# Performance work log

Hardware: AMD Instinct MI355X
Metric: run time of the kernel (lower is better)

## Reference

```python
import jax, jax.numpy as jnp
import numpy as np

N_NODES = 50000
N_EDGES = 1_600_000
F_IN = 128
F_OUT = 8
K_TAPS = 4
AVG_DEG = 32.0


def setup_inputs() -> dict:
    key = jax.random.key(0)
    k1, k2, k3, k4, k5 = jax.random.split(key, 5)
    x = jax.random.normal(k1, (N_NODES, F_IN), dtype=jnp.float32)
    gso_rows = jax.random.randint(k2, (N_EDGES,), 0, N_NODES, dtype=jnp.int32)
    gso_cols = jax.random.randint(k3, (N_EDGES,), 0, N_NODES, dtype=jnp.int32)
    gso_vals = jax.random.uniform(k4, (N_EDGES,), dtype=jnp.float32) / AVG_DEG
    # filterCoeff = randn(outFeat, filter_order) * 0.1 as in torch __init__
    coeff = jax.random.normal(k5, (F_OUT, K_TAPS), dtype=jnp.float32) * 0.1
    return {"x": x, "gso_rows": gso_rows, "gso_cols": gso_cols,
            "gso_vals": gso_vals, "coeff": coeff}


def reference(x, gso_rows, gso_cols, gso_vals, coeff):
    # Faithful to the torch code INCLUDING its carried-over SpMV state:
    # output feature o uses powers S^{1+o(K-1)} .. S^{o(K-1)+K} of x.
    F_out, K = coeff.shape
    N = x.shape[0]
    max_power = F_out * (K - 1) + 1  # highest S power needed

    def spmv(Z):  # S @ Z via edge-list gather + segment_sum scatter
        return jax.ops.segment_sum(gso_vals[:, None] * Z[gso_cols], gso_rows,
                                   num_segments=N)

    def step(Z, _):
        Zn = spmv(Z)
        return Zn, Zn.sum(axis=1)  # sum over in-features done up-front

    # s[p-1, n] = sum_f (S^p x)[n, f], for p = 1..max_power
    _, s = jax.lax.scan(step, x, None, length=max_power)  # (max_power, N)

    # power index (0-based into s) used by output o, tap i: o*(K-1) + i
    idx = jnp.arange(F_out)[:, None] * (K - 1) + jnp.arange(K)[None, :]  # (F_out, K)
    sg = s[idx]  # (F_out, K, N)
    y = jnp.einsum('ok,okn->no', coeff, sg)  # (N, F_out)
    return y
```

## Files before the change

kernel.cpp:

```cpp
#include <hip/hip_runtime.h>
#include <hip/hip_bf16.h>

#define N_NODES 50000
#define N_EDGES 1600000
#define F_IN    128
#define F_OUT   8
#define K_TAPS  4
#define MAX_POWER 25

#define NBLK    256
#define RPB     196
#define CHUNK   4096
#define NPART   391
#define ECAP_G  8192
#define ECAP_L  6912

#define BAR_LINES 16
#define LSTRIDE   32

__device__ inline int wave_incl_scan(int v, int lane) {
    #pragma unroll
    for (int off = 1; off < 64; off <<= 1) {
        int t = __shfl_up(v, off, 64);
        if (lane >= off) v += t;
    }
    return v;
}

__device__ inline void st_coh(float* p, float v) {
    __hip_atomic_store(p, v, __ATOMIC_RELAXED, __HIP_MEMORY_SCOPE_AGENT);
}

__global__ void partition_kernel(const int* __restrict__ rows,
                                 const int* __restrict__ cols,
                                 const float* __restrict__ vals,
                                 int* __restrict__ gcnt,
                                 int2* __restrict__ edges, int n_edges) {
    __shared__ int lhist[NBLK];
    __shared__ int lcur[NBLK];
    __shared__ int lbase[NBLK];
    __shared__ int2 stage[CHUNK];
    __shared__ unsigned char sbkt[CHUNK];
    __shared__ int wsum[4];
    int tid = threadIdx.x;
    int base = blockIdx.x * CHUNK;
    int cend = min(base + CHUNK, n_edges);

    lhist[tid] = 0;
    __syncthreads();
    for (int i = base + tid; i < cend; i += 256)
        atomicAdd(&lhist[rows[i] / RPB], 1);
    __syncthreads();

    int lane = tid & 63, wid = tid >> 6;
    int h = lhist[tid];
    int incl = wave_incl_scan(h, lane);
    if (lane == 63) wsum[wid] = incl;
    __syncthreads();
    int woff = 0;
    for (int w = 0; w < wid; ++w) woff += wsum[w];
    int excl = woff + incl - h;
    lcur[tid] = excl;
    if (h) {
        int g = atomicAdd(&gcnt[tid], h);
        lbase[tid] = tid * ECAP_G + g - excl;
    }
    __syncthreads();

    for (int i = base + tid; i < cend; i += 256) {
        int r = rows[i], c = cols[i];
        float v = vals[i];
        int b = r / RPB;
        int pos = atomicAdd(&lcur[b], 1);
        stage[pos] = make_int2(((r - b * RPB) << 16) | c, __float_as_int(v));
        sbkt[pos] = (unsigned char)b;
    }
    __syncthreads();

    int cn = cend - base;
    for (int i = tid; i < cn; i += 256) {
        int b = sbkt[i];
        int o = lbase[b] + i;
        if (o - b * ECAP_G < ECAP_G)
            edges[o] = stage[i];
    }
}

__device__ inline void gbar(int it, int b,
                            int* __restrict__ bar_cnt,
                            int* __restrict__ bar_master,
                            int* __restrict__ bar_gen) {
    __syncthreads();
    if (threadIdx.x == 0) {
        int r = b & (BAR_LINES - 1);
        const int need = NBLK / BAR_LINES;
        int c = __hip_atomic_fetch_add(&bar_cnt[(it * BAR_LINES + r) * LSTRIDE], 1,
                                       __ATOMIC_RELAXED, __HIP_MEMORY_SCOPE_AGENT);
        if (c == need - 1) {
            int m = __hip_atomic_fetch_add(&bar_master[it * LSTRIDE], 1,
                                           __ATOMIC_RELAXED, __HIP_MEMORY_SCOPE_AGENT);
            if (m == BAR_LINES - 1)
                __hip_atomic_store(bar_gen, it + 1,
                                   __ATOMIC_RELAXED, __HIP_MEMORY_SCOPE_AGENT);
        }
        while (__hip_atomic_load(bar_gen, __ATOMIC_RELAXED,
                                 __HIP_MEMORY_SCOPE_AGENT) < it + 1)
            __builtin_amdgcn_s_sleep(2);
    }
    __syncthreads();
}

__global__ __launch_bounds__(512, 1)
void chain_kernel(const int* __restrict__ gcnt,
                  const int2* __restrict__ edges,
                  const float* __restrict__ x,
                  const float* __restrict__ coeff,
                  float* __restrict__ u,
                  float* __restrict__ s,
                  float* __restrict__ y,
                  int* __restrict__ bar_cnt,
                  int* __restrict__ bar_master,
                  int* __restrict__ bar_gen,
                  int n_nodes) {
    __shared__ int2  ecache[ECAP_L];
    __shared__ float acc[RPB];
    __shared__ float yacc[RPB * F_OUT];
    __shared__ float lcoeff[F_OUT * K_TAPS];

    int tid = threadIdx.x;
    int b = blockIdx.x;

    if (tid < RPB) acc[tid] = 0.f;
    for (int j = tid; j < RPB * F_OUT; j += 512) yacc[j] = 0.f;
    if (tid < F_OUT * K_TAPS) lcoeff[tid] = coeff[tid];

    int cnt = min(gcnt[b], ECAP_G);
    int cntl = min(cnt, ECAP_L);
    const int2* eb = edges + (size_t)b * ECAP_G;
    for (int i = tid; i < cntl; i += 512) ecache[i] = eb[i];

    {
        int lane = tid & 63;
        int wave = (b * 512 + tid) >> 6;
        int n_waves = NBLK * 8;
        for (int node = wave; node < n_nodes; node += n_waves) {
            const float2* xp = (const float2*)(x + (size_t)node * F_IN);
            float2 v = xp[lane];
            float sm = v.x + v.y;
            #pragma unroll
            for (int off = 32; off > 0; off >>= 1)
                sm += __shfl_down(sm, off, 64);
            if (lane == 0) st_coh(&u[node], sm);
        }
    }
    gbar(0, b, bar_cnt, bar_master, bar_gen);

    for (int p = 0; p < MAX_POWER; ++p) {
        const float* __restrict__ src = (p == 0) ? u : s + (size_t)(p - 1) * n_nodes;
        float* dst = s + (size_t)p * n_nodes;

        int i = tid;
        for (; i + 3 * 512 < cntl; i += 4 * 512) {
            int2 e0 = ecache[i];
            int2 e1 = ecache[i + 512];
            int2 e2 = ecache[i + 1024];
            int2 e3 = ecache[i + 1536];
            float v0 = src[e0.x & 0xFFFF];
            float v1 = src[e1.x & 0xFFFF];
            float v2 = src[e2.x & 0xFFFF];
            float v3 = src[e3.x & 0xFFFF];
            atomicAdd(&acc[e0.x >> 16], __int_as_float(e0.y) * v0);
            atomicAdd(&acc[e1.x >> 16], __int_as_float(e1.y) * v1);
            atomicAdd(&acc[e2.x >> 16], __int_as_float(e2.y) * v2);
            atomicAdd(&acc[e3.x >> 16], __int_as_float(e3.y) * v3);
        }
        for (; i < cntl; i += 512) {
            int2 ev = ecache[i];
            atomicAdd(&acc[ev.x >> 16], __int_as_float(ev.y) * src[ev.x & 0xFFFF]);
        }
        for (int k = ECAP_L + tid; k < cnt; k += 512) {
            int2 ev = eb[k];
            atomicAdd(&acc[ev.x >> 16], __int_as_float(ev.y) * src[ev.x & 0xFFFF]);
        }
        __syncthreads();

        if (tid < RPB) {
            int row = b * RPB + tid;
            float val = acc[tid];
            acc[tid] = 0.f;
            if (p < MAX_POWER - 1 && row < n_nodes) st_coh(&dst[row], val);
            #pragma unroll
            for (int o = 0; o < F_OUT; ++o) {
                int k = p - (K_TAPS - 1) * o;
                if (k >= 0 && k < K_TAPS)
                    yacc[tid * F_OUT + o] += lcoeff[o * K_TAPS + k] * val;
            }
        }
        if (p < MAX_POWER - 1)
            gbar(p + 1, b, bar_cnt, bar_master, bar_gen);
    }

    __syncthreads();
    for (int j = tid; j < RPB * F_OUT; j += 512) {
        int row = b * RPB + (j >> 3);
        if (row < n_nodes) y[(size_t)row * F_OUT + (j & 7)] = yacc[j];
    }
}

extern "C" void kernel_launch(void* const* d_in, const int* in_sizes, int n_in,
                              void* d_out, int out_size, void* d_ws, size_t ws_size,
                              hipStream_t stream) {
    const float* x        = (const float*)d_in[0];
    const int*   gso_rows = (const int*)d_in[1];
    const int*   gso_cols = (const int*)d_in[2];
    const float* gso_vals = (const float*)d_in[3];
    const float* coeff    = (const float*)d_in[4];
    float* y = (float*)d_out;

    float* u     = (float*)d_ws;
    float* s     = u + N_NODES;
    int2*  edges = (int2*)(s + (size_t)MAX_POWER * N_NODES);
    int*   gcnt       = (int*)(edges + (size_t)NBLK * ECAP_G);
    int*   bar_cnt    = gcnt + NBLK;
    int*   bar_master = bar_cnt + MAX_POWER * BAR_LINES * LSTRIDE;
    int*   bar_gen    = bar_master + MAX_POWER * LSTRIDE;

    size_t ctrl_ints = (size_t)NBLK + MAX_POWER * BAR_LINES * LSTRIDE
                     + MAX_POWER * LSTRIDE + 1;
    hipMemsetAsync(gcnt, 0, ctrl_ints * sizeof(int), stream);

    partition_kernel<<<NPART, 256, 0, stream>>>(
        gso_rows, gso_cols, gso_vals, gcnt, edges, N_EDGES);

    int n_nodes = N_NODES;
    void* args[] = { (void*)&gcnt, (void*)&edges, (void*)&x, (void*)&coeff,
                     (void*)&u, (void*)&s, (void*)&y,
                     (void*)&bar_cnt, (void*)&bar_master, (void*)&bar_gen,
                     (void*)&n_nodes };
    hipLaunchCooperativeKernel((void*)chain_kernel, dim3(NBLK), dim3(512),
                               args, 0, stream);
}
```

Baseline: 424.7 us.

## Replace hierarchical counter barrier with per-block flag barrier and sort edges by column

```diff
diff --git a/kernel.cpp b/kernel.cpp
--- a/kernel.cpp
+++ b/kernel.cpp
@@ -14,9 +14,9 @@
 #define NPART   391
 #define ECAP_G  8192
 #define ECAP_L  6912
-
-#define BAR_LINES 16
-#define LSTRIDE   32
+#define CSB     800
+
+#define FSTRIDE 16
 
 __device__ inline int wave_incl_scan(int v, int lane) {
     #pragma unroll
@@ -86,25 +86,14 @@
     }
 }
 
-__device__ inline void gbar(int it, int b,
-                            int* __restrict__ bar_cnt,
-                            int* __restrict__ bar_master,
-                            int* __restrict__ bar_gen) {
-    __syncthreads();
-    if (threadIdx.x == 0) {
-        int r = b & (BAR_LINES - 1);
-        const int need = NBLK / BAR_LINES;
-        int c = __hip_atomic_fetch_add(&bar_cnt[(it * BAR_LINES + r) * LSTRIDE], 1,
-                                       __ATOMIC_RELAXED, __HIP_MEMORY_SCOPE_AGENT);
-        if (c == need - 1) {
-            int m = __hip_atomic_fetch_add(&bar_master[it * LSTRIDE], 1,
-                                           __ATOMIC_RELAXED, __HIP_MEMORY_SCOPE_AGENT);
-            if (m == BAR_LINES - 1)
-                __hip_atomic_store(bar_gen, it + 1,
-                                   __ATOMIC_RELAXED, __HIP_MEMORY_SCOPE_AGENT);
-        }
-        while (__hip_atomic_load(bar_gen, __ATOMIC_RELAXED,
-                                 __HIP_MEMORY_SCOPE_AGENT) < it + 1)
+__device__ inline void gbar(int gen, int* __restrict__ flags) {
+    __syncthreads();
+    if (threadIdx.x == 0)
+        __hip_atomic_store(&flags[blockIdx.x * FSTRIDE], gen,
+                           __ATOMIC_RELAXED, __HIP_MEMORY_SCOPE_AGENT);
+    if (threadIdx.x < NBLK) {
+        while (__hip_atomic_load(&flags[threadIdx.x * FSTRIDE],
+                                 __ATOMIC_RELAXED, __HIP_MEMORY_SCOPE_AGENT) < gen)
             __builtin_amdgcn_s_sleep(2);
     }
     __syncthreads();
@@ -118,11 +107,12 @@
                   float* __restrict__ u,
                   float* __restrict__ s,
                   float* __restrict__ y,
-                  int* __restrict__ bar_cnt,
-                  int* __restrict__ bar_master,
-                  int* __restrict__ bar_gen,
+                  int* __restrict__ flags,
                   int n_nodes) {
-    __shared__ int2  ecache[ECAP_L];
+    __shared__ int2  esort[ECAP_L];
+    __shared__ int   chist[CSB];
+    __shared__ int   ccur[CSB];
+    __shared__ int   wsum8[8];
     __shared__ float acc[RPB];
     __shared__ float yacc[RPB * F_OUT];
     __shared__ float lcoeff[F_OUT * K_TAPS];
@@ -137,7 +127,37 @@
     int cnt = min(gcnt[b], ECAP_G);
     int cntl = min(cnt, ECAP_L);
     const int2* eb = edges + (size_t)b * ECAP_G;
-    for (int i = tid; i < cntl; i += 512) ecache[i] = eb[i];
+
+    for (int i = tid; i < CSB; i += 512) chist[i] = 0;
+    __syncthreads();
+    if (cnt <= ECAP_L) {
+        for (int i = tid; i < cnt; i += 512) {
+            int2 e = eb[i];
+            atomicAdd(&chist[(e.x & 0xFFFF) >> 6], 1);
+        }
+        __syncthreads();
+        int lane = tid & 63, wid = tid >> 6;
+        int b0 = 2 * tid;
+        int h0 = (b0 < CSB) ? chist[b0] : 0;
+        int h1 = (b0 + 1 < CSB) ? chist[b0 + 1] : 0;
+        int ps = h0 + h1;
+        int incl = wave_incl_scan(ps, lane);
+        if (lane == 63) wsum8[wid] = incl;
+        __syncthreads();
+        int woff = 0;
+        for (int w = 0; w < wid; ++w) woff += wsum8[w];
+        int ex = woff + incl - ps;
+        if (b0 < CSB) ccur[b0] = ex;
+        if (b0 + 1 < CSB) ccur[b0 + 1] = ex + h0;
+        __syncthreads();
+        for (int i = tid; i < cnt; i += 512) {
+            int2 e = eb[i];
+            int pos = atomicAdd(&ccur[(e.x & 0xFFFF) >> 6], 1);
+            esort[pos] = e;
+        }
+    } else {
+        for (int i = tid; i < cntl; i += 512) esort[i] = eb[i];
+    }
 
     {
         int lane = tid & 63;
@@ -153,7 +173,7 @@
             if (lane == 0) st_coh(&u[node], sm);
         }
     }
-    gbar(0, b, bar_cnt, bar_master, bar_gen);
+    gbar(1, flags);
 
     for (int p = 0; p < MAX_POWER; ++p) {
         const float* __restrict__ src = (p == 0) ? u : s + (size_t)(p - 1) * n_nodes;
@@ -161,10 +181,10 @@
 
         int i = tid;
         for (; i + 3 * 512 < cntl; i += 4 * 512) {
-            int2 e0 = ecache[i];
-            int2 e1 = ecache[i + 512];
-            int2 e2 = ecache[i + 1024];
-            int2 e3 = ecache[i + 1536];
+            int2 e0 = esort[i];
+            int2 e1 = esort[i + 512];
+            int2 e2 = esort[i + 1024];
+            int2 e3 = esort[i + 1536];
             float v0 = src[e0.x & 0xFFFF];
             float v1 = src[e1.x & 0xFFFF];
             float v2 = src[e2.x & 0xFFFF];
@@ -175,7 +195,7 @@
             atomicAdd(&acc[e3.x >> 16], __int_as_float(e3.y) * v3);
         }
         for (; i < cntl; i += 512) {
-            int2 ev = ecache[i];
+            int2 ev = esort[i];
             atomicAdd(&acc[ev.x >> 16], __int_as_float(ev.y) * src[ev.x & 0xFFFF]);
         }
         for (int k = ECAP_L + tid; k < cnt; k += 512) {
@@ -197,7 +217,7 @@
             }
         }
         if (p < MAX_POWER - 1)
-            gbar(p + 1, b, bar_cnt, bar_master, bar_gen);
+            gbar(p + 2, flags);
     }
 
     __syncthreads();
@@ -220,13 +240,10 @@
     float* u     = (float*)d_ws;
     float* s     = u + N_NODES;
     int2*  edges = (int2*)(s + (size_t)MAX_POWER * N_NODES);
-    int*   gcnt       = (int*)(edges + (size_t)NBLK * ECAP_G);
-    int*   bar_cnt    = gcnt + NBLK;
-    int*   bar_master = bar_cnt + MAX_POWER * BAR_LINES * LSTRIDE;
-    int*   bar_gen    = bar_master + MAX_POWER * LSTRIDE;
-
-    size_t ctrl_ints = (size_t)NBLK + MAX_POWER * BAR_LINES * LSTRIDE
-                     + MAX_POWER * LSTRIDE + 1;
+    int*   gcnt  = (int*)(edges + (size_t)NBLK * ECAP_G);
+    int*   flags = gcnt + NBLK;
+
+    size_t ctrl_ints = (size_t)NBLK + (size_t)NBLK * FSTRIDE;
     hipMemsetAsync(gcnt, 0, ctrl_ints * sizeof(int), stream);
 
     partition_kernel<<<NPART, 256, 0, stream>>>(
@@ -234,8 +251,7 @@
 
     int n_nodes = N_NODES;
     void* args[] = { (void*)&gcnt, (void*)&edges, (void*)&x, (void*)&coeff,
-                     (void*)&u, (void*)&s, (void*)&y,
-                     (void*)&bar_cnt, (void*)&bar_master, (void*)&bar_gen,
+                     (void*)&u, (void*)&s, (void*)&y, (void*)&flags,
                      (void*)&n_nodes };
     hipLaunchCooperativeKernel((void*)chain_kernel, dim3(NBLK), dim3(512),
                                args, 0, stream);
```

After: 411.0 us. -3.2%, faster.
